# Optimization experiments

Measured on AMD Instinct MI355X. Metric: run time of the kernel, lower is better.

## Reference

```python
import jax, jax.numpy as jnp
import numpy as np

B, N, A, M, D = 64, 128, 64, 128, 64  # batch, in_caps, in_dim, out_caps, out_dim
SCALE = 1.0 / np.sqrt(D).astype(np.float32)
W_INIT = np.sqrt(M / (A * N)).astype(np.float32)


def setup_inputs() -> dict:
    key = jax.random.key(0)
    k1, k2, k3, k4, k5 = jax.random.split(key, 5)
    return {
        "input": jax.random.normal(k1, (B, N, A), dtype=jnp.float32),
        "current_act": jax.random.uniform(k2, (B, N), dtype=jnp.float32),
        "next_capsule_value": jax.random.normal(k3, (B, M, D), dtype=jnp.float32),
        "next_act": jax.random.uniform(k4, (B, M), dtype=jnp.float32),
        "w": W_INIT * jax.random.normal(k5, (N, A, M, D), dtype=jnp.float32),
        "num_iter": 1,
    }


def reference(input, current_act, next_capsule_value, next_act, w, num_iter):
    # Per-(input-capsule, output-capsule) votes: bna,namd->bnmd (shared by both einsums)
    votes = jnp.einsum('bna,namd->bnmd', input, w)
    # Routing logits: agreement between votes and current output poses
    logits = jnp.einsum('bnmd,bmd->bnm', votes, next_capsule_value) * SCALE
    qk = jax.nn.softmax(logits, axis=2)
    # Modulate by next-layer activations and renormalize over output capsules
    qk = qk * next_act[:, None, :]
    qk = qk / (jnp.sum(qk, axis=2, keepdims=True) + 1e-10)
    # Weighted aggregation of votes, gated by input-capsule activations
    ncv = jnp.einsum('bnm,bnmd,bn->bmd', qk, votes, current_act)
    # act_type == 'ONES'; dropout rate 0.0 (identity); nonlinear_act is identity
    na = jnp.ones(ncv.shape[:2], dtype=ncv.dtype)
    return ncv, na, qk
```

## Files before the change

kernel.cpp:

```cpp
#include <hip/hip_runtime.h>

typedef __attribute__((ext_vector_type(8))) short bf16x8;
typedef __attribute__((ext_vector_type(4))) float f32x4;

constexpr int Bq = 64, Nq = 128, Aq = 64, Mq = 128, Dq = 64;
constexpr int MD = Mq * Dq;
constexpr int NM = Nq * Mq;
constexpr int NA = Nq * Aq;
constexpr int NCV_SZ = Bq * MD;
constexpr int NA_SZ  = Bq * Mq;
constexpr float SCALE = 0.125f;

__device__ __forceinline__ unsigned short f2b(float f) {
  unsigned u = __float_as_uint(f);
  return (unsigned short)((u + 0x7fffu + ((u >> 16) & 1u)) >> 16);
}
__device__ __forceinline__ unsigned cvt2(float lo, float hi) {
  return ((unsigned)f2b(hi) << 16) | (unsigned)f2b(lo);
}
__device__ __forceinline__ bf16x8 pack8(const float* v) {
  union { unsigned u[4]; bf16x8 b; } x;
  x.u[0] = cvt2(v[0], v[1]); x.u[1] = cvt2(v[2], v[3]);
  x.u[2] = cvt2(v[4], v[5]); x.u[3] = cvt2(v[6], v[7]);
  return x.b;
}
__device__ __forceinline__ void dma16(const float* g, float* l) {
  __builtin_amdgcn_global_load_lds(
      (const __attribute__((address_space(1))) unsigned*)g,
      (__attribute__((address_space(3))) unsigned*)l, 16, 0, 0);
}

__global__ __launch_bounds__(256) void k0_init(float* __restrict__ out) {
  int i = blockIdx.x * 256 + threadIdx.x;
  if (i < NCV_SZ) out[i] = 0.0f;
  else if (i < NCV_SZ + NA_SZ) out[i] = 1.0f;
}

__global__ __launch_bounds__(512, 2) void k1_logits(
    const float* __restrict__ input, const float* __restrict__ ncvin,
    const float* __restrict__ wgt, float* __restrict__ logits) {
  const int mc = blockIdx.x;
  const int n0 = blockIdx.y * 16;
  const int t = threadIdx.x;
  const int w8 = t >> 6, l = t & 63;
  const int wv_m = w8 & 3, wv_b = w8 >> 2;
  const int lr = l & 15, g = l >> 4;
  const int m = mc * 4 + wv_m;
  __shared__ float Wf[4][32 * 256];

  float cnv[2][4][4];
#pragma unroll
  for (int i = 0; i < 2; ++i)
#pragma unroll
    for (int j = 0; j < 4; ++j)
#pragma unroll
      for (int r = 0; r < 4; ++r)
        cnv[i][j][r] = ncvin[(size_t)(32 * wv_b + 16 * i + 4 * g + r) * MD + m * Dq + 16 * j + lr];

  auto stageT = [&](int h) {
    if (h > 31) return;
    const int hh = 31 - h;
    const int nn = n0 + (hh >> 1);
    const int ks = (hh & 1) * 32;
    float* dst = &Wf[h & 3][0];
#pragma unroll
    for (int rr = 0; rr < 4; ++rr) {
      const int al = w8 * 4 + rr;
      const char* gs = (const char*)(wgt + (size_t)(nn * Aq + ks + al) * MD + mc * 256)
                       + ((l * 16) ^ (((al >> 3) & 1) << 6));
      dma16((const float*)gs, dst + al * 256);
    }
  };
  auto loadAv = [&](int h, float (&av)[2][8]) {
    if (h > 31) return;
    const int hh = 31 - h;
    const int nn = n0 + (hh >> 1);
    const int ks = (hh & 1) * 32;
#pragma unroll
    for (int i = 0; i < 2; ++i) {
      const float* ap = input + (size_t)(32 * wv_b + 16 * i + lr) * NA + nn * Aq + ks + g * 8;
      *(float4*)&av[i][0] = *(const float4*)ap;
      *(float4*)&av[i][4] = *(const float4*)(ap + 4);
    }
  };
  auto mfmaPhase = [&](int h, float (&av)[2][8], f32x4 (&acc)[2][4]) {
    bf16x8 af[2];
#pragma unroll
    for (int i = 0; i < 2; ++i) af[i] = pack8(av[i]);
    const float* bufp = &Wf[h & 3][0];
#pragma unroll
    for (int j = 0; j < 4; ++j) {
      const int cx = (64 * wv_m + 16 * j + lr) ^ ((g & 1) << 4);
      float bv[8];
#pragma unroll
      for (int e = 0; e < 8; ++e) bv[e] = bufp[(g * 8 + e) * 256 + cx];
      bf16x8 bf = pack8(bv);
#pragma unroll
      for (int i = 0; i < 2; ++i)
        acc[i][j] = __builtin_amdgcn_mfma_f32_16x16x32_bf16(af[i], bf, acc[i][j], 0, 0, 0);
    }
  };

  float avE[2][8], avO[2][8];
  stageT(0);
  loadAv(0, avE);
  stageT(1);
  stageT(2);

  f32x4 acc[2][4];
  for (int hp = 0; hp < 16; ++hp) {
    const int h0 = hp * 2, h1 = h0 + 1;
    if (hp == 0)      asm volatile("s_waitcnt vmcnt(8)" ::: "memory");
    else if (hp < 15) asm volatile("s_waitcnt vmcnt(4)" ::: "memory");
    else              asm volatile("s_waitcnt vmcnt(0)" ::: "memory");
    __builtin_amdgcn_s_barrier();
#pragma unroll
    for (int i = 0; i < 2; ++i)
#pragma unroll
      for (int j = 0; j < 4; ++j) acc[i][j] = (f32x4)(0.0f);
    mfmaPhase(h0, avE, acc);
    __builtin_amdgcn_sched_barrier(0);
    loadAv(h1, avO);
    __builtin_amdgcn_sched_barrier(0);
    stageT(h0 + 3);
    if (hp < 15) asm volatile("s_waitcnt vmcnt(4)" ::: "memory");
    else         asm volatile("s_waitcnt vmcnt(0)" ::: "memory");
    __builtin_amdgcn_s_barrier();
    mfmaPhase(h1, avO, acc);
    {
      const int nn = n0 + ((31 - h1) >> 1);
      float lp[2][4];
#pragma unroll
      for (int i = 0; i < 2; ++i)
#pragma unroll
        for (int r = 0; r < 4; ++r) lp[i][r] = 0.0f;
#pragma unroll
      for (int i = 0; i < 2; ++i)
#pragma unroll
        for (int j = 0; j < 4; ++j)
#pragma unroll
          for (int r = 0; r < 4; ++r)
            lp[i][r] = fmaf(acc[i][j][r], cnv[i][j][r], lp[i][r]);
#pragma unroll
      for (int off = 1; off < 16; off <<= 1)
#pragma unroll
        for (int i = 0; i < 2; ++i)
#pragma unroll
          for (int r = 0; r < 4; ++r) lp[i][r] += __shfl_xor(lp[i][r], off);
      float ov = lp[0][0];
#pragma unroll
      for (int i = 0; i < 2; ++i)
#pragma unroll
        for (int r = 0; r < 4; ++r)
          ov = (lr == i * 4 + r) ? lp[i][r] : ov;
      if (lr < 8) {
        const int b = 32 * wv_b + 16 * (lr >> 2) + 4 * g + (lr & 3);
        logits[(size_t)b * NM + (size_t)nn * Mq + m] = SCALE * ov;
      }
    }
    __builtin_amdgcn_sched_barrier(0);
    loadAv(h0 + 2, avE);
    __builtin_amdgcn_sched_barrier(0);
    stageT(h1 + 3);
  }
}

__global__ __launch_bounds__(256) void k2_softmax(
    const float* __restrict__ next_act, float* __restrict__ qk) {
  const int row  = blockIdx.x * 4 + (threadIdx.x >> 6);
  const int lane = threadIdx.x & 63;
  const int b = row >> 7;
  float* p = qk + (size_t)row * Mq;
  float x0 = p[lane], x1 = p[lane + 64];
  float mx = fmaxf(x0, x1);
#pragma unroll
  for (int off = 32; off; off >>= 1) mx = fmaxf(mx, __shfl_xor(mx, off));
  float e0 = __expf(x0 - mx), e1 = __expf(x1 - mx);
  float s = e0 + e1;
#pragma unroll
  for (int off = 32; off; off >>= 1) s += __shfl_xor(s, off);
  float a0 = next_act[b * Mq + lane], a1 = next_act[b * Mq + lane + 64];
  float t0 = (e0 / s) * a0, t1 = (e1 / s) * a1;
  float s2 = t0 + t1;
#pragma unroll
  for (int off = 32; off; off >>= 1) s2 += __shfl_xor(s2, off);
  s2 += 1e-10f;
  p[lane]      = t0 / s2;
  p[lane + 64] = t1 / s2;
}

__global__ __launch_bounds__(512, 2) void k3_aggregate(
    const float* __restrict__ input, const float* __restrict__ cur_act,
    const float* __restrict__ wgt, const float* __restrict__ qk,
    float* __restrict__ ncv) {
  const int mc = blockIdx.x;
  const int n0 = blockIdx.y * 16;
  const int t = threadIdx.x;
  const int w8 = t >> 6, l = t & 63;
  const int wv_m = w8 & 3, wv_b = w8 >> 2;
  const int lr = l & 15, g = l >> 4;
  const int m = mc * 4 + wv_m;
  __shared__ float Wf[4][32 * 256];
  __shared__ float zl[16][4][64];

#pragma unroll
  for (int p = 0; p < 2; ++p) {
    const int idx = t + p * 512;
    const int b = idx >> 4, nn = idx & 15;
    float4 q4 = *(const float4*)&qk[(size_t)b * NM + (size_t)(n0 + nn) * Mq + mc * 4];
    float ca = cur_act[b * Nq + n0 + nn];
    zl[nn][0][b] = q4.x * ca; zl[nn][1][b] = q4.y * ca;
    zl[nn][2][b] = q4.z * ca; zl[nn][3][b] = q4.w * ca;
  }
  __syncthreads();

  auto stageT = [&](int h) {
    if (h > 31) return;
    const int nn = n0 + (h >> 1);
    const int ks = (h & 1) * 32;
    float* dst = &Wf[h & 3][0];
#pragma unroll
    for (int rr = 0; rr < 4; ++rr) {
      const int al = w8 * 4 + rr;
      const char* gs = (const char*)(wgt + (size_t)(nn * Aq + ks + al) * MD + mc * 256)
                       + ((l * 16) ^ (((al >> 3) & 1) << 6));
      dma16((const float*)gs, dst + al * 256);
    }
  };
  auto loadAv = [&](int h, float (&av)[2][8]) {
    if (h > 31) return;
    const int nn = n0 + (h >> 1);
    const int ks = (h & 1) * 32;
#pragma unroll
    for (int i = 0; i < 2; ++i) {
      const float* ap = input + (size_t)(32 * wv_b + 16 * i + lr) * NA + nn * Aq + ks + g * 8;
      *(float4*)&av[i][0] = *(const float4*)ap;
      *(float4*)&av[i][4] = *(const float4*)(ap + 4);
    }
  };
  auto mfmaPhase = [&](int h, float (&av)[2][8], float (&zr)[2], f32x4 (&acc)[2][4]) {
    bf16x8 af[2];
#pragma unroll
    for (int i = 0; i < 2; ++i) {
      float sv[8];
#pragma unroll
      for (int e = 0; e < 8; ++e) sv[e] = av[i][e] * zr[i];
      af[i] = pack8(sv);
    }
    const float* bufp = &Wf[h & 3][0];
#pragma unroll
    for (int j = 0; j < 4; ++j) {
      const int cx = (64 * wv_m + 16 * j + lr) ^ ((g & 1) << 4);
      float bv[8];
#pragma unroll
      for (int e = 0; e < 8; ++e) bv[e] = bufp[(g * 8 + e) * 256 + cx];
      bf16x8 bf = pack8(bv);
#pragma unroll
      for (int i = 0; i < 2; ++i)
        acc[i][j] = __builtin_amdgcn_mfma_f32_16x16x32_bf16(af[i], bf, acc[i][j], 0, 0, 0);
    }
  };

  float avE[2][8], avO[2][8];
  stageT(0);
  loadAv(0, avE);
  stageT(1);
  stageT(2);

  f32x4 acc[2][4];
#pragma unroll
  for (int i = 0; i < 2; ++i)
#pragma unroll
    for (int j = 0; j < 4; ++j) acc[i][j] = (f32x4)(0.0f);

  float zr[2];
  for (int hp = 0; hp < 16; ++hp) {
    const int h0 = hp * 2, h1 = h0 + 1;
    if (hp == 0)      asm volatile("s_waitcnt vmcnt(8)" ::: "memory");
    else if (hp < 15) asm volatile("s_waitcnt vmcnt(4)" ::: "memory");
    else              asm volatile("s_waitcnt vmcnt(0)" ::: "memory");
    __builtin_amdgcn_s_barrier();
#pragma unroll
    for (int i = 0; i < 2; ++i) zr[i] = zl[hp][wv_m][32 * wv_b + 16 * i + lr];
    mfmaPhase(h0, avE, zr, acc);
    __builtin_amdgcn_sched_barrier(0);
    loadAv(h1, avO);
    __builtin_amdgcn_sched_barrier(0);
    stageT(h0 + 3);
    if (hp < 15) asm volatile("s_waitcnt vmcnt(4)" ::: "memory");
    else         asm volatile("s_waitcnt vmcnt(0)" ::: "memory");
    __builtin_amdgcn_s_barrier();
    mfmaPhase(h1, avO, zr, acc);
    __builtin_amdgcn_sched_barrier(0);
    loadAv(h0 + 2, avE);
    __builtin_amdgcn_sched_barrier(0);
    stageT(h1 + 3);
  }

#pragma unroll
  for (int i = 0; i < 2; ++i)
#pragma unroll
    for (int j = 0; j < 4; ++j) {
      const int d = 16 * j + lr;
#pragma unroll
      for (int r = 0; r < 4; ++r) {
        const int b = 32 * wv_b + 16 * i + 4 * g + r;
        atomicAdd(&ncv[(size_t)b * MD + m * Dq + d], acc[i][j][r]);
      }
    }
}

extern "C" void kernel_launch(void* const* d_in, const int* in_sizes, int n_in,
                              void* d_out, int out_size, void* d_ws, size_t ws_size,
                              hipStream_t stream) {
  const float* input    = (const float*)d_in[0];
  const float* cur_act  = (const float*)d_in[1];
  const float* ncvin    = (const float*)d_in[2];
  const float* next_act = (const float*)d_in[3];
  const float* wgt      = (const float*)d_in[4];

  float* out = (float*)d_out;
  float* ncv = out;
  float* qk  = out + NCV_SZ + NA_SZ;

  k0_init<<<(NCV_SZ + NA_SZ + 255) / 256, 256, 0, stream>>>(out);
  k1_logits<<<dim3(32, 8), 512, 0, stream>>>(input, ncvin, wgt, qk);
  k2_softmax<<<(Bq * Nq) / 4, 256, 0, stream>>>(next_act, qk);
  k3_aggregate<<<dim3(32, 8), 512, 0, stream>>>(input, cur_act, wgt, qk, ncv);
}
```

Measured before the change: 161.0 us.

## Warp-specialize logits and aggregate kernels with dedicated DMA producer waves

Both main kernels grow from 8 to 12 waves per block. The 4 extra waves only issue global-to-LDS DMA loads of the weight tiles into a 4-deep ring buffer. The 8 original waves only load activations and run MFMA, handing buffers off through paired barriers. The aim is to take weight staging and its vmcnt waits off the compute waves' critical path so loads overlap matrix math better. The cost is more threads per block and lockstep barriers between producers and consumers, which may limit occupancy or add stalls.

```diff
diff --git a/kernel.cpp b/kernel.cpp
--- a/kernel.cpp
+++ b/kernel.cpp
@@ -36,132 +36,133 @@
   else if (i < NCV_SZ + NA_SZ) out[i] = 1.0f;
 }
 
-__global__ __launch_bounds__(512, 2) void k1_logits(
+__global__ __launch_bounds__(768, 3) void k1_logits(
     const float* __restrict__ input, const float* __restrict__ ncvin,
     const float* __restrict__ wgt, float* __restrict__ logits) {
   const int mc = blockIdx.x;
   const int n0 = blockIdx.y * 16;
   const int t = threadIdx.x;
-  const int w8 = t >> 6, l = t & 63;
-  const int wv_m = w8 & 3, wv_b = w8 >> 2;
-  const int lr = l & 15, g = l >> 4;
-  const int m = mc * 4 + wv_m;
+  const int w = t >> 6, l = t & 63;
   __shared__ float Wf[4][32 * 256];
 
-  float cnv[2][4][4];
-#pragma unroll
-  for (int i = 0; i < 2; ++i)
-#pragma unroll
-    for (int j = 0; j < 4; ++j)
-#pragma unroll
-      for (int r = 0; r < 4; ++r)
-        cnv[i][j][r] = ncvin[(size_t)(32 * wv_b + 16 * i + 4 * g + r) * MD + m * Dq + 16 * j + lr];
-
-  auto stageT = [&](int h) {
-    if (h > 31) return;
-    const int hh = 31 - h;
-    const int nn = n0 + (hh >> 1);
-    const int ks = (hh & 1) * 32;
-    float* dst = &Wf[h & 3][0];
-#pragma unroll
-    for (int rr = 0; rr < 4; ++rr) {
-      const int al = w8 * 4 + rr;
-      const char* gs = (const char*)(wgt + (size_t)(nn * Aq + ks + al) * MD + mc * 256)
-                       + ((l * 16) ^ (((al >> 3) & 1) << 6));
-      dma16((const float*)gs, dst + al * 256);
-    }
-  };
-  auto loadAv = [&](int h, float (&av)[2][8]) {
-    if (h > 31) return;
-    const int hh = 31 - h;
-    const int nn = n0 + (hh >> 1);
-    const int ks = (hh & 1) * 32;
-#pragma unroll
-    for (int i = 0; i < 2; ++i) {
-      const float* ap = input + (size_t)(32 * wv_b + 16 * i + lr) * NA + nn * Aq + ks + g * 8;
-      *(float4*)&av[i][0] = *(const float4*)ap;
-      *(float4*)&av[i][4] = *(const float4*)(ap + 4);
-    }
-  };
-  auto mfmaPhase = [&](int h, float (&av)[2][8], f32x4 (&acc)[2][4]) {
-    bf16x8 af[2];
-#pragma unroll
-    for (int i = 0; i < 2; ++i) af[i] = pack8(av[i]);
-    const float* bufp = &Wf[h & 3][0];
-#pragma unroll
-    for (int j = 0; j < 4; ++j) {
-      const int cx = (64 * wv_m + 16 * j + lr) ^ ((g & 1) << 4);
-      float bv[8];
-#pragma unroll
-      for (int e = 0; e < 8; ++e) bv[e] = bufp[(g * 8 + e) * 256 + cx];
-      bf16x8 bf = pack8(bv);
-#pragma unroll
-      for (int i = 0; i < 2; ++i)
-        acc[i][j] = __builtin_amdgcn_mfma_f32_16x16x32_bf16(af[i], bf, acc[i][j], 0, 0, 0);
-    }
-  };
-
-  float avE[2][8], avO[2][8];
-  stageT(0);
-  loadAv(0, avE);
-  stageT(1);
-  stageT(2);
-
-  f32x4 acc[2][4];
-  for (int hp = 0; hp < 16; ++hp) {
-    const int h0 = hp * 2, h1 = h0 + 1;
-    if (hp == 0)      asm volatile("s_waitcnt vmcnt(8)" ::: "memory");
-    else if (hp < 15) asm volatile("s_waitcnt vmcnt(4)" ::: "memory");
-    else              asm volatile("s_waitcnt vmcnt(0)" ::: "memory");
-    __builtin_amdgcn_s_barrier();
+  if (w >= 8) {
+    const int pw = w - 8;
+    auto stageT = [&](int h) {
+      const int hh = 31 - h;
+      const int nn = n0 + (hh >> 1);
+      const int ks = (hh & 1) * 32;
+      float* dst = &Wf[h & 3][0];
+#pragma unroll
+      for (int rr = 0; rr < 8; ++rr) {
+        const int al = pw * 8 + rr;
+        const char* gs = (const char*)(wgt + (size_t)(nn * Aq + ks + al) * MD + mc * 256)
+                         + ((l * 16) ^ (((al >> 3) & 1) << 6));
+        dma16((const float*)gs, dst + al * 256);
+      }
+    };
+    stageT(0); stageT(1); stageT(2); stageT(3);
+    for (int h = 0; h < 32; ++h) {
+      if (h <= 28)      asm volatile("s_waitcnt vmcnt(24)" ::: "memory");
+      else if (h == 29) asm volatile("s_waitcnt vmcnt(16)" ::: "memory");
+      else if (h == 30) asm volatile("s_waitcnt vmcnt(8)"  ::: "memory");
+      else              asm volatile("s_waitcnt vmcnt(0)"  ::: "memory");
+      __builtin_amdgcn_s_barrier();
+      __builtin_amdgcn_s_barrier();
+      if (h + 4 < 32) stageT(h + 4);
+    }
+  } else {
+    const int wv_m = w & 3, wv_b = w >> 2;
+    const int lr = l & 15, g = l >> 4;
+    const int m = mc * 4 + wv_m;
+
+    float cnv[2][4][4];
 #pragma unroll
     for (int i = 0; i < 2; ++i)
 #pragma unroll
-      for (int j = 0; j < 4; ++j) acc[i][j] = (f32x4)(0.0f);
-    mfmaPhase(h0, avE, acc);
-    __builtin_amdgcn_sched_barrier(0);
-    loadAv(h1, avO);
-    __builtin_amdgcn_sched_barrier(0);
-    stageT(h0 + 3);
-    if (hp < 15) asm volatile("s_waitcnt vmcnt(4)" ::: "memory");
-    else         asm volatile("s_waitcnt vmcnt(0)" ::: "memory");
-    __builtin_amdgcn_s_barrier();
-    mfmaPhase(h1, avO, acc);
-    {
-      const int nn = n0 + ((31 - h1) >> 1);
-      float lp[2][4];
-#pragma unroll
-      for (int i = 0; i < 2; ++i)
-#pragma unroll
-        for (int r = 0; r < 4; ++r) lp[i][r] = 0.0f;
-#pragma unroll
-      for (int i = 0; i < 2; ++i)
-#pragma unroll
-        for (int j = 0; j < 4; ++j)
-#pragma unroll
-          for (int r = 0; r < 4; ++r)
-            lp[i][r] = fmaf(acc[i][j][r], cnv[i][j][r], lp[i][r]);
-#pragma unroll
-      for (int off = 1; off < 16; off <<= 1)
+      for (int j = 0; j < 4; ++j)
+#pragma unroll
+        for (int r = 0; r < 4; ++r)
+          cnv[i][j][r] = ncvin[(size_t)(32 * wv_b + 16 * i + 4 * g + r) * MD + m * Dq + 16 * j + lr];
+
+    auto loadAv = [&](int h, float (&av)[2][8]) {
+      if (h > 31) return;
+      const int hh = 31 - h;
+      const int nn = n0 + (hh >> 1);
+      const int ks = (hh & 1) * 32;
+#pragma unroll
+      for (int i = 0; i < 2; ++i) {
+        const float* ap = input + (size_t)(32 * wv_b + 16 * i + lr) * NA + nn * Aq + ks + g * 8;
+        *(float4*)&av[i][0] = *(const float4*)ap;
+        *(float4*)&av[i][4] = *(const float4*)(ap + 4);
+      }
+    };
+    auto mfmaPhase = [&](int h, float (&av)[2][8], f32x4 (&acc)[2][4]) {
+      bf16x8 af[2];
+#pragma unroll
+      for (int i = 0; i < 2; ++i) af[i] = pack8(av[i]);
+      const float* bufp = &Wf[h & 3][0];
+#pragma unroll
+      for (int j = 0; j < 4; ++j) {
+        const int cx = (64 * wv_m + 16 * j + lr) ^ ((g & 1) << 4);
+        float bv[8];
+#pragma unroll
+        for (int e = 0; e < 8; ++e) bv[e] = bufp[(g * 8 + e) * 256 + cx];
+        bf16x8 bf = pack8(bv);
 #pragma unroll
         for (int i = 0; i < 2; ++i)
-#pragma unroll
-          for (int r = 0; r < 4; ++r) lp[i][r] += __shfl_xor(lp[i][r], off);
-      float ov = lp[0][0];
-#pragma unroll
-      for (int i = 0; i < 2; ++i)
-#pragma unroll
-        for (int r = 0; r < 4; ++r)
-          ov = (lr == i * 4 + r) ? lp[i][r] : ov;
-      if (lr < 8) {
-        const int b = 32 * wv_b + 16 * (lr >> 2) + 4 * g + (lr & 3);
-        logits[(size_t)b * NM + (size_t)nn * Mq + m] = SCALE * ov;
-      }
-    }
-    __builtin_amdgcn_sched_barrier(0);
-    loadAv(h0 + 2, avE);
-    __builtin_amdgcn_sched_barrier(0);
-    stageT(h1 + 3);
+          acc[i][j] = __builtin_amdgcn_mfma_f32_16x16x32_bf16(af[i], bf, acc[i][j], 0, 0, 0);
+      }
+    };
+
+    float avE[2][8], avO[2][8];
+    loadAv(0, avE);
+    f32x4 acc[2][4];
+    for (int h = 0; h < 32; ++h) {
+      __builtin_amdgcn_s_barrier();
+      if ((h & 1) == 0) {
+#pragma unroll
+        for (int i = 0; i < 2; ++i)
+#pragma unroll
+          for (int j = 0; j < 4; ++j) acc[i][j] = (f32x4)(0.0f);
+        loadAv(h + 1, avO);
+        mfmaPhase(h, avE, acc);
+      } else {
+        loadAv(h + 1, avE);
+        mfmaPhase(h, avO, acc);
+        {
+          const int nn = n0 + ((31 - h) >> 1);
+          float lp[2][4];
+#pragma unroll
+          for (int i = 0; i < 2; ++i)
+#pragma unroll
+            for (int r = 0; r < 4; ++r) lp[i][r] = 0.0f;
+#pragma unroll
+          for (int i = 0; i < 2; ++i)
+#pragma unroll
+            for (int j = 0; j < 4; ++j)
+#pragma unroll
+              for (int r = 0; r < 4; ++r)
+                lp[i][r] = fmaf(acc[i][j][r], cnv[i][j][r], lp[i][r]);
+#pragma unroll
+          for (int off = 1; off < 16; off <<= 1)
+#pragma unroll
+            for (int i = 0; i < 2; ++i)
+#pragma unroll
+              for (int r = 0; r < 4; ++r) lp[i][r] += __shfl_xor(lp[i][r], off);
+          float ov = lp[0][0];
+#pragma unroll
+          for (int i = 0; i < 2; ++i)
+#pragma unroll
+            for (int r = 0; r < 4; ++r)
+              ov = (lr == i * 4 + r) ? lp[i][r] : ov;
+          if (lr < 8) {
+            const int b = 32 * wv_b + 16 * (lr >> 2) + 4 * g + (lr & 3);
+            logits[(size_t)b * NM + (size_t)nn * Mq + m] = SCALE * ov;
+          }
+        }
+      }
+      __builtin_amdgcn_s_barrier();
+    }
   }
 }
 
@@ -189,125 +190,126 @@
   p[lane + 64] = t1 / s2;
 }
 
-__global__ __launch_bounds__(512, 2) void k3_aggregate(
+__global__ __launch_bounds__(768, 3) void k3_aggregate(
     const float* __restrict__ input, const float* __restrict__ cur_act,
     const float* __restrict__ wgt, const float* __restrict__ qk,
     float* __restrict__ ncv) {
   const int mc = blockIdx.x;
   const int n0 = blockIdx.y * 16;
   const int t = threadIdx.x;
-  const int w8 = t >> 6, l = t & 63;
-  const int wv_m = w8 & 3, wv_b = w8 >> 2;
-  const int lr = l & 15, g = l >> 4;
-  const int m = mc * 4 + wv_m;
+  const int w = t >> 6, l = t & 63;
   __shared__ float Wf[4][32 * 256];
   __shared__ float zl[16][4][64];
 
-#pragma unroll
-  for (int p = 0; p < 2; ++p) {
-    const int idx = t + p * 512;
-    const int b = idx >> 4, nn = idx & 15;
-    float4 q4 = *(const float4*)&qk[(size_t)b * NM + (size_t)(n0 + nn) * Mq + mc * 4];
-    float ca = cur_act[b * Nq + n0 + nn];
-    zl[nn][0][b] = q4.x * ca; zl[nn][1][b] = q4.y * ca;
-    zl[nn][2][b] = q4.z * ca; zl[nn][3][b] = q4.w * ca;
+  if (w >= 8) {
+    const int pw = w - 8;
+    auto stageT = [&](int h) {
+      const int nn = n0 + (h >> 1);
+      const int ks = (h & 1) * 32;
+      float* dst = &Wf[h & 3][0];
+#pragma unroll
+      for (int rr = 0; rr < 8; ++rr) {
+        const int al = pw * 8 + rr;
+        const char* gs = (const char*)(wgt + (size_t)(nn * Aq + ks + al) * MD + mc * 256)
+                         + ((l * 16) ^ (((al >> 3) & 1) << 6));
+        dma16((const float*)gs, dst + al * 256);
+      }
+    };
+    stageT(0); stageT(1); stageT(2); stageT(3);
+    for (int h = 0; h < 32; ++h) {
+      if (h <= 28)      asm volatile("s_waitcnt vmcnt(24)" ::: "memory");
+      else if (h == 29) asm volatile("s_waitcnt vmcnt(16)" ::: "memory");
+      else if (h == 30) asm volatile("s_waitcnt vmcnt(8)"  ::: "memory");
+      else              asm volatile("s_waitcnt vmcnt(0)"  ::: "memory");
+      __builtin_amdgcn_s_barrier();
+      __builtin_amdgcn_s_barrier();
+      if (h + 4 < 32) stageT(h + 4);
+    }
+  } else {
+    const int wv_m = w & 3, wv_b = w >> 2;
+    const int lr = l & 15, g = l >> 4;
+    const int m = mc * 4 + wv_m;
+
+#pragma unroll
+    for (int p = 0; p < 2; ++p) {
+      const int idx = w * 64 + l + p * 512;
+      const int b = idx >> 4, nn = idx & 15;
+      float4 q4 = *(const float4*)&qk[(size_t)b * NM + (size_t)(n0 + nn) * Mq + mc * 4];
+      float ca = cur_act[b * Nq + n0 + nn];
+      zl[nn][0][b] = q4.x * ca; zl[nn][1][b] = q4.y * ca;
+      zl[nn][2][b] = q4.z * ca; zl[nn][3][b] = q4.w * ca;
+    }
+    asm volatile("s_waitcnt lgkmcnt(0)" ::: "memory");
+
+    auto loadAv = [&](int h, float (&av)[2][8]) {
+      if (h > 31) return;
+      const int nn = n0 + (h >> 1);
+      const int ks = (h & 1) * 32;
+#pragma unroll
+      for (int i = 0; i < 2; ++i) {
+        const float* ap = input + (size_t)(32 * wv_b + 16 * i + lr) * NA + nn * Aq + ks + g * 8;
+        *(float4*)&av[i][0] = *(const float4*)ap;
+        *(float4*)&av[i][4] = *(const float4*)(ap + 4);
+      }
+    };
+    auto mfmaPhase = [&](int h, float (&av)[2][8], float (&zr)[2], f32x4 (&acc)[2][4]) {
+      bf16x8 af[2];
+#pragma unroll
+      for (int i = 0; i < 2; ++i) {
+        float sv[8];
+#pragma unroll
+        for (int e = 0; e < 8; ++e) sv[e] = av[i][e] * zr[i];
+        af[i] = pack8(sv);
+      }
+      const float* bufp = &Wf[h & 3][0];
+#pragma unroll
+      for (int j = 0; j < 4; ++j) {
+        const int cx = (64 * wv_m + 16 * j + lr) ^ ((g & 1) << 4);
+        float bv[8];
+#pragma unroll
+        for (int e = 0; e < 8; ++e) bv[e] = bufp[(g * 8 + e) * 256 + cx];
+        bf16x8 bf = pack8(bv);
+#pragma unroll
+        for (int i = 0; i < 2; ++i)
+          acc[i][j] = __builtin_amdgcn_mfma_f32_16x16x32_bf16(af[i], bf, acc[i][j], 0, 0, 0);
+      }
+    };
+
+    float avE[2][8], avO[2][8];
+    loadAv(0, avE);
+    f32x4 acc[2][4];
+#pragma unroll
+    for (int i = 0; i < 2; ++i)
+#pragma unroll
+      for (int j = 0; j < 4; ++j) acc[i][j] = (f32x4)(0.0f);
+
+    float zr[2];
+    for (int h = 0; h < 32; ++h) {
+      __builtin_amdgcn_s_barrier();
+      if ((h & 1) == 0) {
+#pragma unroll
+        for (int i = 0; i < 2; ++i) zr[i] = zl[h >> 1][wv_m][32 * wv_b + 16 * i + lr];
+        loadAv(h + 1, avO);
+        mfmaPhase(h, avE, zr, acc);
+      } else {
+        loadAv(h + 1, avE);
+        mfmaPhase(h, avO, zr, acc);
+      }
+      __builtin_amdgcn_s_barrier();
+    }
+
+#pragma unroll
+    for (int i = 0; i < 2; ++i)
+#pragma unroll
+      for (int j = 0; j < 4; ++j) {
+        const int d = 16 * j + lr;
+#pragma unroll
+        for (int r = 0; r < 4; ++r) {
+          const int b = 32 * wv_b + 16 * i + 4 * g + r;
+          atomicAdd(&ncv[(size_t)b * MD + m * Dq + d], acc[i][j][r]);
+        }
+      }
   }
-  __syncthreads();
-
-  auto stageT = [&](int h) {
-    if (h > 31) return;
-    const int nn = n0 + (h >> 1);
-    const int ks = (h & 1) * 32;
-    float* dst = &Wf[h & 3][0];
-#pragma unroll
-    for (int rr = 0; rr < 4; ++rr) {
-      const int al = w8 * 4 + rr;
-      const char* gs = (const char*)(wgt + (size_t)(nn * Aq + ks + al) * MD + mc * 256)
-                       + ((l * 16) ^ (((al >> 3) & 1) << 6));
-      dma16((const float*)gs, dst + al * 256);
-    }
-  };
-  auto loadAv = [&](int h, float (&av)[2][8]) {
-    if (h > 31) return;
-    const int nn = n0 + (h >> 1);
-    const int ks = (h & 1) * 32;
-#pragma unroll
-    for (int i = 0; i < 2; ++i) {
-      const float* ap = input + (size_t)(32 * wv_b + 16 * i + lr) * NA + nn * Aq + ks + g * 8;
-      *(float4*)&av[i][0] = *(const float4*)ap;
-      *(float4*)&av[i][4] = *(const float4*)(ap + 4);
-    }
-  };
-  auto mfmaPhase = [&](int h, float (&av)[2][8], float (&zr)[2], f32x4 (&acc)[2][4]) {
-    bf16x8 af[2];
-#pragma unroll
-    for (int i = 0; i < 2; ++i) {
-      float sv[8];
-#pragma unroll
-      for (int e = 0; e < 8; ++e) sv[e] = av[i][e] * zr[i];
-      af[i] = pack8(sv);
-    }
-    const float* bufp = &Wf[h & 3][0];
-#pragma unroll
-    for (int j = 0; j < 4; ++j) {
-      const int cx = (64 * wv_m + 16 * j + lr) ^ ((g & 1) << 4);
-      float bv[8];
-#pragma unroll
-      for (int e = 0; e < 8; ++e) bv[e] = bufp[(g * 8 + e) * 256 + cx];
-      bf16x8 bf = pack8(bv);
-#pragma unroll
-      for (int i = 0; i < 2; ++i)
-        acc[i][j] = __builtin_amdgcn_mfma_f32_16x16x32_bf16(af[i], bf, acc[i][j], 0, 0, 0);
-    }
-  };
-
-  float avE[2][8], avO[2][8];
-  stageT(0);
-  loadAv(0, avE);
-  stageT(1);
-  stageT(2);
-
-  f32x4 acc[2][4];
-#pragma unroll
-  for (int i = 0; i < 2; ++i)
-#pragma unroll
-    for (int j = 0; j < 4; ++j) acc[i][j] = (f32x4)(0.0f);
-
-  float zr[2];
-  for (int hp = 0; hp < 16; ++hp) {
-    const int h0 = hp * 2, h1 = h0 + 1;
-    if (hp == 0)      asm volatile("s_waitcnt vmcnt(8)" ::: "memory");
-    else if (hp < 15) asm volatile("s_waitcnt vmcnt(4)" ::: "memory");
-    else              asm volatile("s_waitcnt vmcnt(0)" ::: "memory");
-    __builtin_amdgcn_s_barrier();
-#pragma unroll
-    for (int i = 0; i < 2; ++i) zr[i] = zl[hp][wv_m][32 * wv_b + 16 * i + lr];
-    mfmaPhase(h0, avE, zr, acc);
-    __builtin_amdgcn_sched_barrier(0);
-    loadAv(h1, avO);
-    __builtin_amdgcn_sched_barrier(0);
-    stageT(h0 + 3);
-    if (hp < 15) asm volatile("s_waitcnt vmcnt(4)" ::: "memory");
-    else         asm volatile("s_waitcnt vmcnt(0)" ::: "memory");
-    __builtin_amdgcn_s_barrier();
-    mfmaPhase(h1, avO, zr, acc);
-    __builtin_amdgcn_sched_barrier(0);
-    loadAv(h0 + 2, avE);
-    __builtin_amdgcn_sched_barrier(0);
-    stageT(h1 + 3);
-  }
-
-#pragma unroll
-  for (int i = 0; i < 2; ++i)
-#pragma unroll
-    for (int j = 0; j < 4; ++j) {
-      const int d = 16 * j + lr;
-#pragma unroll
-      for (int r = 0; r < 4; ++r) {
-        const int b = 32 * wv_b + 16 * i + 4 * g + r;
-        atomicAdd(&ncv[(size_t)b * MD + m * Dq + d], acc[i][j][r]);
-      }
-    }
 }
 
 extern "C" void kernel_launch(void* const* d_in, const int* in_sizes, int n_in,
@@ -324,7 +326,7 @@
   float* qk  = out + NCV_SZ + NA_SZ;
 
   k0_init<<<(NCV_SZ + NA_SZ + 255) / 256, 256, 0, stream>>>(out);
-  k1_logits<<<dim3(32, 8), 512, 0, stream>>>(input, ncvin, wgt, qk);
+  k1_logits<<<dim3(32, 8), 768, 0, stream>>>(input, ncvin, wgt, qk);
   k2_softmax<<<(Bq * Nq) / 4, 256, 0, stream>>>(next_act, qk);
-  k3_aggregate<<<dim3(32, 8), 512, 0, stream>>>(input, cur_act, wgt, qk, ncv);
-}
+  k3_aggregate<<<dim3(32, 8), 768, 0, stream>>>(input, cur_act, wgt, qk, ncv);
+}
```

Result: faster. 147.5 us (-8.4%).
